# Optimization experiments

Measured on AMD Instinct MI355X. Metric: run time of the kernel, lower is better.

Reference implementation:

```python
import jax, jax.numpy as jnp
import numpy as np

HEADS = 4
DIM_HEAD = 32
GROUPS = 32  # min(256//4, 32)
EPS = 1e-5


def setup_inputs() -> dict:
    key = jax.random.key(0)
    ks = jax.random.split(key, 5)
    B, C, H, W = 16, 256, 64, 64
    CD, HC, WC = 512, 32, 32
    hid = HEADS * DIM_HEAD  # 128
    return {
        "x": jax.random.normal(ks[0], (B, C, H, W), jnp.float32),
        "cond": jax.random.normal(ks[1], (B, CD, HC, WC), jnp.float32),
        "gn_w": jnp.ones((C,), jnp.float32),
        "gn_b": jnp.zeros((C,), jnp.float32),
        "w_q": jax.random.normal(ks[2], (hid, C), jnp.float32) * 0.05,
        "b_q": jnp.zeros((hid,), jnp.float32),
        "w_kv": jax.random.normal(ks[3], (2 * hid, CD), jnp.float32) * 0.05,
        "b_kv": jnp.zeros((2 * hid,), jnp.float32),
        "w_out": jax.random.normal(ks[4], (C, hid), jnp.float32) * 0.05,
        "b_out": jnp.zeros((C,), jnp.float32),
    }


def _group_norm(x, w, b):
    # x: (B, C, H, W); normalize per group over (channels-in-group, H, W)
    B, C, H, W = x.shape
    xg = x.reshape(B, GROUPS, C // GROUPS, H, W)
    mu = jnp.mean(xg, axis=(2, 3, 4), keepdims=True)
    var = jnp.var(xg, axis=(2, 3, 4), keepdims=True)
    xn = ((xg - mu) * jax.lax.rsqrt(var + EPS)).reshape(B, C, H, W)
    return xn * w[None, :, None, None] + b[None, :, None, None]


def _conv1x1(x, w, b):
    # x: (B, Cin, H, W), w: (Cout, Cin), b: (Cout,)
    return jnp.einsum('oc,bchw->bohw', w, x) + b[None, :, None, None]


def reference(x, cond, gn_w, gn_b, w_q, b_q, w_kv, b_kv, w_out, b_out):
    B, C, H, W = x.shape
    hid = HEADS * DIM_HEAD
    xn = _group_norm(x, gn_w, gn_b)
    q = _conv1x1(xn, w_q, b_q)          # (B, hid, H, W)
    kv = _conv1x1(cond, w_kv, b_kv)     # (B, 2*hid, Hc, Wc)
    Nc = kv.shape[2] * kv.shape[3]
    N = H * W
    k = kv[:, :hid].reshape(B, HEADS, DIM_HEAD, Nc)
    v = kv[:, hid:].reshape(B, HEADS, DIM_HEAD, Nc)
    q = q.reshape(B, HEADS, DIM_HEAD, N)
    k = jax.nn.softmax(k, axis=-1)
    # kv outer product: (B, heads, d, e)
    context = jnp.einsum('bhdn,bhen->bhde', k, v)
    # query contraction over d: (B, heads, e, n)
    out = jnp.einsum('bhde,bhdn->bhen', context, q)
    out = out.reshape(B, hid, H, W)
    return _conv1x1(out, w_out, b_out)
```

## Files before the change

kernel.cpp:

```cpp
#include <hip/hip_runtime.h>
#include <hip/hip_bf16.h>

typedef __attribute__((ext_vector_type(8))) short bf16x8;
typedef __attribute__((ext_vector_type(4))) float f32x4;

__device__ __forceinline__ ushort f2bf(float f) {
    __hip_bfloat16 h = __float2bfloat16(f);
    return __builtin_bit_cast(ushort, h);
}
__device__ __forceinline__ unsigned pack2(float a, float b) {
    return (unsigned)f2bf(a) | ((unsigned)f2bf(b) << 16);
}
__device__ __forceinline__ float bflo(unsigned u) { return __uint_as_float(u << 16); }

__global__ __launch_bounds__(512) void kvctx_kernel(const float* __restrict__ w_kv,
                                                    const float* __restrict__ cond,
                                                    const float* __restrict__ b_kv,
                                                    const float* __restrict__ x,
                                                    float* __restrict__ statacc,
                                                    float* __restrict__ rsp,
                                                    float* __restrict__ ctxp) {
    __shared__ ushort lA[256 * 64];
    __shared__ ushort lB[64 * 64];
    __shared__ float scratch[64 * 64];
    __shared__ float red[16];
    int bid = blockIdx.x, t = threadIdx.x;
    if (bid < 256) {
        int b = bid >> 4, nc = bid & 15;
        int col0 = nc * 64;
        int l = t & 63, w = t >> 6;
        int lr = l & 15, lg = l >> 4;
        const float* Bb = cond + (size_t)b * 512 * 1024 + col0;
        int rA = t >> 3, gAr = t & 7, gw = gAr ^ (rA & 7);
        int rB = t >> 4, gB = t & 15;
        int sp = t & 31, sj4 = t >> 5;
        float4 ka0_, ka1_, ka2_, ka3_, ka4_, ka5_, ka6_, ka7_;
        float4 kb0_, kb1_;
#define KC_LOADA(k0) { \
    ka0_ = *(const float4*)&w_kv[(size_t)(rA)       * 512 + (k0) + gAr * 8]; \
    ka1_ = *(const float4*)&w_kv[(size_t)(rA)       * 512 + (k0) + gAr * 8 + 4]; \
    ka2_ = *(const float4*)&w_kv[(size_t)(64 + rA)  * 512 + (k0) + gAr * 8]; \
    ka3_ = *(const float4*)&w_kv[(size_t)(64 + rA)  * 512 + (k0) + gAr * 8 + 4]; \
    ka4_ = *(const float4*)&w_kv[(size_t)(128 + rA) * 512 + (k0) + gAr * 8]; \
    ka5_ = *(const float4*)&w_kv[(size_t)(128 + rA) * 512 + (k0) + gAr * 8 + 4]; \
    ka6_ = *(const float4*)&w_kv[(size_t)(192 + rA) * 512 + (k0) + gAr * 8]; \
    ka7_ = *(const float4*)&w_kv[(size_t)(192 + rA) * 512 + (k0) + gAr * 8 + 4]; }
#define KC_LOADB(k0) { \
    kb0_ = *(const float4*)&Bb[(size_t)((k0) + rB)      * 1024 + gB * 4]; \
    kb1_ = *(const float4*)&Bb[(size_t)((k0) + 32 + rB) * 1024 + gB * 4]; }
#define KC_WRITEA() { uint4 p; \
    p.x = pack2(ka0_.x, ka0_.y); p.y = pack2(ka0_.z, ka0_.w); \
    p.z = pack2(ka1_.x, ka1_.y); p.w = pack2(ka1_.z, ka1_.w); \
    *(uint4*)((char*)lA + (size_t)((rA)       * 8 + gw) * 16) = p; \
    p.x = pack2(ka2_.x, ka2_.y); p.y = pack2(ka2_.z, ka2_.w); \
    p.z = pack2(ka3_.x, ka3_.y); p.w = pack2(ka3_.z, ka3_.w); \
    *(uint4*)((char*)lA + (size_t)((64 + rA)  * 8 + gw) * 16) = p; \
    p.x = pack2(ka4_.x, ka4_.y); p.y = pack2(ka4_.z, ka4_.w); \
    p.z = pack2(ka5_.x, ka5_.y); p.w = pack2(ka5_.z, ka5_.w); \
    *(uint4*)((char*)lA + (size_t)((128 + rA) * 8 + gw) * 16) = p; \
    p.x = pack2(ka6_.x, ka6_.y); p.y = pack2(ka6_.z, ka6_.w); \
    p.z = pack2(ka7_.x, ka7_.y); p.w = pack2(ka7_.z, ka7_.w); \
    *(uint4*)((char*)lA + (size_t)((192 + rA) * 8 + gw) * 16) = p; }
#define KC_WRITEB() { \
    *(float4*)((char*)scratch + (rB)      * 256 + ((gB ^ (((rB)      >> 1) & 15)) * 16)) = kb0_; \
    *(float4*)((char*)scratch + (32 + rB) * 256 + ((gB ^ (((32 + rB) >> 1) & 15)) * 16)) = kb1_; }
#define KC_PACKB() { \
    int swz = sp & 15; \
    float4 s0 = *(const float4*)((char*)scratch + (2*sp)   * 256 + ((sj4 ^ swz) * 16)); \
    float4 s2 = *(const float4*)((char*)scratch + (2*sp+1) * 256 + ((sj4 ^ swz) * 16)); \
    float c0v[4] = {s0.x, s0.y, s0.z, s0.w}; \
    float c1v[4] = {s2.x, s2.y, s2.z, s2.w}; \
    _Pragma("unroll") \
    for (int w4 = 0; w4 < 4; ++w4) { \
        int n = sj4 * 4 + w4; \
        unsigned pk = pack2(c0v[w4], c1v[w4]); \
        *(unsigned*)((char*)lB + n * 128 + (((sp >> 2) ^ (n & 7)) * 16) + (sp & 3) * 4) = pk; \
    } }
        KC_LOADA(0); KC_LOADB(0);
        f32x4 acc[2][4] = {};
        for (int it = 0; it < 8; ++it) {
            KC_WRITEA();
            KC_WRITEB();
            __syncthreads();
            if (it < 7) { KC_LOADA(it * 64 + 64); KC_LOADB(it * 64 + 64); }
            KC_PACKB();
            __syncthreads();
            #pragma unroll
            for (int ks = 0; ks < 2; ++ks) {
                bf16x8 av[2], bv[4];
                #pragma unroll
                for (int mi = 0; mi < 2; ++mi) {
                    int ar = w * 32 + mi * 16 + lr;
                    int q = (ks * 4 + lg) ^ (ar & 7);
                    av[mi] = *(const bf16x8*)((const char*)lA + ar * 128 + q * 16);
                }
                #pragma unroll
                for (int ni = 0; ni < 4; ++ni) {
                    int br = ni * 16 + lr;
                    int q = (ks * 4 + lg) ^ (br & 7);
                    bv[ni] = *(const bf16x8*)((const char*)lB + br * 128 + q * 16);
                }
                #pragma unroll
                for (int mi = 0; mi < 2; ++mi)
                    #pragma unroll
                    for (int ni = 0; ni < 4; ++ni)
                        acc[mi][ni] = __builtin_amdgcn_mfma_f32_16x16x32_bf16(
                            av[mi], bv[ni], acc[mi][ni], 0, 0, 0);
            }
            __syncthreads();
        }
#undef KC_LOADA
#undef KC_LOADB
#undef KC_WRITEA
#undef KC_WRITEB
#undef KC_PACKB
        bool isK = (w < 4);
        float bk[2][4];
        #pragma unroll
        for (int mi = 0; mi < 2; ++mi)
            #pragma unroll
            for (int reg = 0; reg < 4; ++reg)
                bk[mi][reg] = b_kv[w * 32 + mi * 16 + lg * 4 + reg];
        float rs[2][4];
        #pragma unroll
        for (int mi = 0; mi < 2; ++mi)
            #pragma unroll
            for (int reg = 0; reg < 4; ++reg) rs[mi][reg] = 0.f;
        #pragma unroll
        for (int mi = 0; mi < 2; ++mi) {
            #pragma unroll
            for (int ni = 0; ni < 4; ++ni) {
                #pragma unroll
                for (int reg = 0; reg < 4; ++reg) {
                    int R = w * 32 + mi * 16 + lg * 4 + reg;
                    int N = ni * 16 + lr;
                    float val = acc[mi][ni][reg] + bk[mi][reg];
                    ushort uo;
                    if (isK) {
                        uo = f2bf(__expf(val));
                        rs[mi][reg] += bflo((unsigned)uo);
                    } else {
                        uo = f2bf(val);
                    }
                    *(ushort*)((char*)lA + R * 128 + (((N >> 3) ^ (R & 7)) * 16) + (N & 7) * 2) = uo;
                }
            }
        }
        if (isK) {
            #pragma unroll
            for (int mi = 0; mi < 2; ++mi) {
                #pragma unroll
                for (int reg = 0; reg < 4; ++reg) {
                    float v = rs[mi][reg];
                    v += __shfl_xor(v, 1, 64);
                    v += __shfl_xor(v, 2, 64);
                    v += __shfl_xor(v, 4, 64);
                    v += __shfl_xor(v, 8, 64);
                    if (lr == 0)
                        rsp[(size_t)(b * 16 + nc) * 128 + w * 32 + mi * 16 + lg * 4 + reg] = v;
                }
            }
        }
        __syncthreads();
        if (isK) {
            f32x4 c00 = {}, c01 = {}, c10 = {}, c11 = {};
            #pragma unroll
            for (int ks = 0; ks < 2; ++ks) {
                int ar0 = w * 32 + lr,        qa0 = (ks * 4 + lg) ^ (ar0 & 7);
                int ar1 = w * 32 + 16 + lr,   qa1 = (ks * 4 + lg) ^ (ar1 & 7);
                int br0 = 128 + w * 32 + lr,      qb0 = (ks * 4 + lg) ^ (br0 & 7);
                int br1 = 128 + w * 32 + 16 + lr, qb1 = (ks * 4 + lg) ^ (br1 & 7);
                bf16x8 pa0 = *(const bf16x8*)((const char*)lA + ar0 * 128 + qa0 * 16);
                bf16x8 pa1 = *(const bf16x8*)((const char*)lA + ar1 * 128 + qa1 * 16);
                bf16x8 pv0 = *(const bf16x8*)((const char*)lA + br0 * 128 + qb0 * 16);
                bf16x8 pv1 = *(const bf16x8*)((const char*)lA + br1 * 128 + qb1 * 16);
                c00 = __builtin_amdgcn_mfma_f32_16x16x32_bf16(pa0, pv0, c00, 0, 0, 0);
                c01 = __builtin_amdgcn_mfma_f32_16x16x32_bf16(pa0, pv1, c01, 0, 0, 0);
                c10 = __builtin_amdgcn_mfma_f32_16x16x32_bf16(pa1, pv0, c10, 0, 0, 0);
                c11 = __builtin_amdgcn_mfma_f32_16x16x32_bf16(pa1, pv1, c11, 0, 0, 0);
            }
            float* cp = ctxp + (size_t)(b * 16 + nc) * 4096 + w * 1024;
            #pragma unroll
            for (int reg = 0; reg < 4; ++reg) {
                int d0 = lg * 4 + reg;
                cp[d0 * 32 + lr]              = c00[reg];
                cp[d0 * 32 + 16 + lr]         = c01[reg];
                cp[(16 + d0) * 32 + lr]       = c10[reg];
                cp[(16 + d0) * 32 + 16 + lr]  = c11[reg];
            }
        }
    } else {
        int bg = bid - 256;
        const float4* xp = (const float4*)(x + (size_t)bg * 32768);
        float s = 0.f, ss = 0.f;
        #pragma unroll
        for (int j = 0; j < 16; ++j) {
            float4 v = xp[t + 512 * j];
            s  += v.x + v.y + v.z + v.w;
            ss += v.x*v.x + v.y*v.y + v.z*v.z + v.w*v.w;
        }
        #pragma unroll
        for (int off = 32; off > 0; off >>= 1) {
            s  += __shfl_down(s, off, 64);
            ss += __shfl_down(ss, off, 64);
        }
        int wave = t >> 6;
        if ((t & 63) == 0) { red[wave * 2] = s; red[wave * 2 + 1] = ss; }
        __syncthreads();
        if (t == 0) {
            float S = 0.f, SS = 0.f;
            #pragma unroll
            for (int i = 0; i < 8; ++i) { S += red[i * 2]; SS += red[i * 2 + 1]; }
            statacc[bg * 2]     = S;
            statacc[bg * 2 + 1] = SS;
        }
    }
}

__global__ __launch_bounds__(256) void a_kernel(const float* __restrict__ ctxp,
                                                const float* __restrict__ rsp,
                                                const float* __restrict__ w_out,
                                                const float* __restrict__ w_q,
                                                const float* __restrict__ b_q,
                                                const float* __restrict__ statacc,
                                                const float* __restrict__ gn_w,
                                                const float* __restrict__ gn_b,
                                                const float* __restrict__ b_out,
                                                ushort* __restrict__ A16,
                                                float* __restrict__ biasb) {
    __shared__ float ctxl[4][32][33];
    __shared__ float wol[16][128];
    __shared__ float ml[16][128];
    __shared__ float cbuf[256][17];
    __shared__ float pbuf[16][17];
    __shared__ float rsinv[128];
    int b = blockIdx.x >> 4, ot = (blockIdx.x & 15) << 4;
    int t = threadIdx.x;
    if (t < 128) {
        float s = 0.f;
        #pragma unroll
        for (int nc = 0; nc < 16; ++nc)
            s += rsp[(size_t)(b * 16 + nc) * 128 + t];
        rsinv[t] = 1.f / s;
    }
    #pragma unroll
    for (int j = 0; j < 8; ++j) {
        int e = t + 256 * j;
        wol[e >> 7][e & 127] = w_out[(ot + (e >> 7)) * 128 + (e & 127)];
    }
    __syncthreads();
    #pragma unroll
    for (int j = 0; j < 16; ++j) {
        int e = t + 256 * j;
        float v = 0.f;
        #pragma unroll
        for (int nc = 0; nc < 16; ++nc)
            v += ctxp[(size_t)(b * 16 + nc) * 4096 + e];
        ctxl[e >> 10][(e >> 5) & 31][e & 31] = v * rsinv[e >> 5];
    }
    __syncthreads();
    #pragma unroll
    for (int j = 0; j < 8; ++j) {
        int e = t + 256 * j;
        int o = e >> 7, hd = e & 127, h = hd >> 5, d = hd & 31;
        float acc = 0.f;
        #pragma unroll
        for (int ee = 0; ee < 32; ++ee) acc += wol[o][h * 32 + ee] * ctxl[h][d][ee];
        ml[o][hd] = acc;
    }
    __syncthreads();
    int c = t, g = c >> 3;
    float a0 = statacc[(b * 32 + g) * 2], a1 = statacc[(b * 32 + g) * 2 + 1];
    float mu  = a0 * (1.f / 32768.f);
    float var = a1 * (1.f / 32768.f) - mu * mu;
    float sc = rsqrtf(var + 1e-5f) * gn_w[c];
    float tc = gn_b[c] - mu * sc;
    float wt[16];
    #pragma unroll
    for (int o = 0; o < 16; ++o) wt[o] = 0.f;
    for (int hd = 0; hd < 128; ++hd) {
        float wq = w_q[hd * 256 + c];
        #pragma unroll
        for (int o = 0; o < 16; ++o) wt[o] += ml[o][hd] * wq;
    }
    ushort* Abp = A16 + ((size_t)b * 256 + ot) * 256 + c;
    #pragma unroll
    for (int o = 0; o < 16; ++o) {
        Abp[(size_t)o * 256] = f2bf(wt[o] * sc);
        cbuf[c][o] = wt[o] * tc;
    }
    __syncthreads();
    {
        int o = t >> 4, seg = t & 15;
        float p = 0.f;
        #pragma unroll
        for (int i = 0; i < 16; ++i) p += cbuf[seg * 16 + i][o];
        pbuf[o][seg] = p;
    }
    __syncthreads();
    if (t < 16) {
        int o = t;
        float sum = 0.f;
        #pragma unroll
        for (int s2 = 0; s2 < 16; ++s2) sum += pbuf[o][s2];
        float md = 0.f;
        #pragma unroll 8
        for (int hd = 0; hd < 128; ++hd) md += ml[o][hd] * b_q[hd];
        biasb[(size_t)b * 256 + ot + o] = sum + md + b_out[ot + o];
    }
}

__global__ __launch_bounds__(512) void out_gemm_fused(const ushort* __restrict__ A16,
                                                      const float* __restrict__ x,
                                                      const float* __restrict__ biasb,
                                                      float* __restrict__ out) {
    __shared__ ushort lA[256 * 64];
    __shared__ ushort lB[128 * 64];
    __shared__ float scratch[64 * 128];
    int b = blockIdx.y;
    int n0 = blockIdx.x * 128;
    int t = threadIdx.x;
    int l = t & 63, wid = t >> 6;
    int wr = wid >> 1, wc = wid & 1;
    int lr = l & 15, lg = l >> 4;
    const ushort* Ab = A16 + (size_t)b * 65536;
    const float* xb = x + (size_t)b * 256 * 4096 + n0;
    int sp = t & 31, sj = t >> 5;
    uint4 a0_, a1_, a2_, a3_;
    float4 b0_, b1_, b2_, b3_;
    int rA = t >> 3, gA = (t & 7) ^ (rA & 7);
    int rB = t >> 5, gB = t & 31;
#define OG_LOADA(k0) { \
    a0_ = *(const uint4*)(Ab + (size_t)(rA)       * 256 + (k0) + gA * 8); \
    a1_ = *(const uint4*)(Ab + (size_t)(64 + rA)  * 256 + (k0) + gA * 8); \
    a2_ = *(const uint4*)(Ab + (size_t)(128 + rA) * 256 + (k0) + gA * 8); \
    a3_ = *(const uint4*)(Ab + (size_t)(192 + rA) * 256 + (k0) + gA * 8); }
#define OG_LOADB(k0) { \
    b0_ = *(const float4*)&xb[(size_t)((k0) + rB)      * 4096 + gB * 4]; \
    b1_ = *(const float4*)&xb[(size_t)((k0) + 16 + rB) * 4096 + gB * 4]; \
    b2_ = *(const float4*)&xb[(size_t)((k0) + 32 + rB) * 4096 + gB * 4]; \
    b3_ = *(const float4*)&xb[(size_t)((k0) + 48 + rB) * 4096 + gB * 4]; }
    OG_LOADA(0); OG_LOADB(0);
    f32x4 acc[4][4] = {};
    for (int it = 0; it < 4; ++it) {
        *(uint4*)((char*)lA + (size_t)t * 16)          = a0_;
        *(uint4*)((char*)lA + (size_t)(512 + t) * 16)  = a1_;
        *(uint4*)((char*)lA + (size_t)(1024 + t) * 16) = a2_;
        *(uint4*)((char*)lA + (size_t)(1536 + t) * 16) = a3_;
        *(float4*)((char*)scratch + (rB)      * 512 + (gB ^ (((rB)      >> 1) & 31)) * 16) = b0_;
        *(float4*)((char*)scratch + (16 + rB) * 512 + (gB ^ (((16 + rB) >> 1) & 31)) * 16) = b1_;
        *(float4*)((char*)scratch + (32 + rB) * 512 + (gB ^ (((32 + rB) >> 1) & 31)) * 16) = b2_;
        *(float4*)((char*)scratch + (48 + rB) * 512 + (gB ^ (((48 + rB) >> 1) & 31)) * 16) = b3_;
        __syncthreads();
        if (it < 3) { OG_LOADA(it * 64 + 64); OG_LOADB(it * 64 + 64); }
        {
            int swz = sp & 31;
            float4 s0 = *(const float4*)((char*)scratch + (2*sp)   * 512 + ((2*sj)   ^ swz) * 16);
            float4 s1 = *(const float4*)((char*)scratch + (2*sp)   * 512 + ((2*sj+1) ^ swz) * 16);
            float4 s2 = *(const float4*)((char*)scratch + (2*sp+1) * 512 + ((2*sj)   ^ swz) * 16);
            float4 s3 = *(const float4*)((char*)scratch + (2*sp+1) * 512 + ((2*sj+1) ^ swz) * 16);
            float c0v[8] = {s0.x, s0.y, s0.z, s0.w, s1.x, s1.y, s1.z, s1.w};
            float c1v[8] = {s2.x, s2.y, s2.z, s2.w, s3.x, s3.y, s3.z, s3.w};
            #pragma unroll
            for (int w = 0; w < 8; ++w) {
                int n = sj * 8 + w;
                unsigned pk = pack2(c0v[w], c1v[w]);
                *(unsigned*)((char*)lB + n * 128 + (((sp >> 2) ^ (n & 7)) * 16) + (sp & 3) * 4) = pk;
            }
        }
        __syncthreads();
        #pragma unroll
        for (int ks = 0; ks < 2; ++ks) {
            bf16x8 av[4], bv[4];
            #pragma unroll
            for (int mi = 0; mi < 4; ++mi) {
                int ar = wr * 64 + mi * 16 + lr;
                int q = (ks * 4 + lg) ^ (ar & 7);
                av[mi] = *(const bf16x8*)((const char*)lA + ar * 128 + q * 16);
            }
            #pragma unroll
            for (int ni = 0; ni < 4; ++ni) {
                int br = wc * 64 + ni * 16 + lr;
                int q = (ks * 4 + lg) ^ (br & 7);
                bv[ni] = *(const bf16x8*)((const char*)lB + br * 128 + q * 16);
            }
            #pragma unroll
            for (int mi = 0; mi < 4; ++mi)
                #pragma unroll
                for (int ni = 0; ni < 4; ++ni)
                    acc[mi][ni] = __builtin_amdgcn_mfma_f32_16x16x32_bf16(
                        av[mi], bv[ni], acc[mi][ni], 0, 0, 0);
        }
        __syncthreads();
    }
#undef OG_LOADA
#undef OG_LOADB
    const float* bp = biasb + (size_t)b * 256;
    int orow = wr * 64, ocol = n0 + wc * 64 + lr;
    #pragma unroll
    for (int mi = 0; mi < 4; ++mi) {
        int rb = orow + mi * 16 + lg * 4;
        float4 b4 = *(const float4*)&bp[rb];
        float bvr[4] = {b4.x, b4.y, b4.z, b4.w};
        #pragma unroll
        for (int ni = 0; ni < 4; ++ni) {
            int cc = ocol + ni * 16;
            #pragma unroll
            for (int r = 0; r < 4; ++r)
                out[((size_t)b * 256 + rb + r) * 4096 + cc] = acc[mi][ni][r] + bvr[r];
        }
    }
}

extern "C" void kernel_launch(void* const* d_in, const int* in_sizes, int n_in,
                              void* d_out, int out_size, void* d_ws, size_t ws_size,
                              hipStream_t stream) {
    const float* x     = (const float*)d_in[0];
    const float* cond  = (const float*)d_in[1];
    const float* gn_w  = (const float*)d_in[2];
    const float* gn_b  = (const float*)d_in[3];
    const float* w_q   = (const float*)d_in[4];
    const float* b_q   = (const float*)d_in[5];
    const float* w_kv  = (const float*)d_in[6];
    const float* b_kv  = (const float*)d_in[7];
    const float* w_out = (const float*)d_in[8];
    const float* b_out = (const float*)d_in[9];
    float* out = (float*)d_out;

    float* f       = (float*)d_ws;
    float* statacc = f;
    float* rsp     = f + 1024;
    float* ctxp    = f + 33792;
    float* biasb   = f + 1082368;
    ushort* A16    = (ushort*)(f + 1086464);

    kvctx_kernel<<<768, 512, 0, stream>>>(w_kv, cond, b_kv, x, statacc, rsp, ctxp);
    a_kernel<<<256, 256, 0, stream>>>(ctxp, rsp, w_out, w_q, b_q, statacc,
                                      gn_w, gn_b, b_out, A16, biasb);
    out_gemm_fused<<<dim3(32, 16), 512, 0, stream>>>(A16, x, biasb, out);
}
```

Before: 77.89 us.

## Fuse group-norm statistics into KV GEMM blocks, interleaving x loads with MFMA loop

The separate 512 group-norm reduction blocks are removed. Each of the 256 KV/context blocks now also streams two groups of x (64K floats), loading x chunks inside the GEMM k-loop and accumulating sum and sum of squares. The aim is to overlap the memory-bound statistics pass with the compute-bound KV GEMM and to cut the grid from 768 to 256 blocks. In exchange, each block carries more registers and memory traffic, and fewer blocks may leave CUs idle or serialise the x reads behind the GEMM.

```diff
diff --git a/kernel.cpp b/kernel.cpp
--- a/kernel.cpp
+++ b/kernel.cpp
@@ -23,19 +23,21 @@
     __shared__ ushort lA[256 * 64];
     __shared__ ushort lB[64 * 64];
     __shared__ float scratch[64 * 64];
-    __shared__ float red[16];
+    __shared__ float red2[8][4];
     int bid = blockIdx.x, t = threadIdx.x;
-    if (bid < 256) {
-        int b = bid >> 4, nc = bid & 15;
-        int col0 = nc * 64;
-        int l = t & 63, w = t >> 6;
-        int lr = l & 15, lg = l >> 4;
-        const float* Bb = cond + (size_t)b * 512 * 1024 + col0;
-        int rA = t >> 3, gAr = t & 7, gw = gAr ^ (rA & 7);
-        int rB = t >> 4, gB = t & 15;
-        int sp = t & 31, sj4 = t >> 5;
-        float4 ka0_, ka1_, ka2_, ka3_, ka4_, ka5_, ka6_, ka7_;
-        float4 kb0_, kb1_;
+    int b = bid >> 4, nc = bid & 15;
+    int col0 = nc * 64;
+    int l = t & 63, w = t >> 6;
+    int lr = l & 15, lg = l >> 4;
+    const float* Bb = cond + (size_t)b * 512 * 1024 + col0;
+    const float4* xc = (const float4*)(x + (size_t)b * 1048576 + (size_t)nc * 65536);
+    int rA = t >> 3, gAr = t & 7, gw = gAr ^ (rA & 7);
+    int rB = t >> 4, gB = t & 15;
+    int sp = t & 31, sj4 = t >> 5;
+    float4 ka0_, ka1_, ka2_, ka3_, ka4_, ka5_, ka6_, ka7_;
+    float4 kb0_, kb1_;
+    float4 xv0_, xv1_, xv2_, xv3_;
+    float sA = 0.f, ssA = 0.f, sB = 0.f, ssB = 0.f;
 #define KC_LOADA(k0) { \
     ka0_ = *(const float4*)&w_kv[(size_t)(rA)       * 512 + (k0) + gAr * 8]; \
     ka1_ = *(const float4*)&w_kv[(size_t)(rA)       * 512 + (k0) + gAr * 8 + 4]; \
@@ -76,144 +78,155 @@
         unsigned pk = pack2(c0v[w4], c1v[w4]); \
         *(unsigned*)((char*)lB + n * 128 + (((sp >> 2) ^ (n & 7)) * 16) + (sp & 3) * 4) = pk; \
     } }
-        KC_LOADA(0); KC_LOADB(0);
-        f32x4 acc[2][4] = {};
-        for (int it = 0; it < 8; ++it) {
-            KC_WRITEA();
-            KC_WRITEB();
-            __syncthreads();
-            if (it < 7) { KC_LOADA(it * 64 + 64); KC_LOADB(it * 64 + 64); }
-            KC_PACKB();
-            __syncthreads();
-            #pragma unroll
-            for (int ks = 0; ks < 2; ++ks) {
-                bf16x8 av[2], bv[4];
+    KC_LOADA(0); KC_LOADB(0);
+    f32x4 acc[2][4] = {};
+    for (int it = 0; it < 8; ++it) {
+        KC_WRITEA();
+        KC_WRITEB();
+        __syncthreads();
+        if (it < 7) { KC_LOADA(it * 64 + 64); KC_LOADB(it * 64 + 64); }
+        xv0_ = xc[t + 512 * (4 * it)];
+        xv1_ = xc[t + 512 * (4 * it + 1)];
+        xv2_ = xc[t + 512 * (4 * it + 2)];
+        xv3_ = xc[t + 512 * (4 * it + 3)];
+        KC_PACKB();
+        __syncthreads();
+        #pragma unroll
+        for (int ks = 0; ks < 2; ++ks) {
+            bf16x8 av[2], bv[4];
+            #pragma unroll
+            for (int mi = 0; mi < 2; ++mi) {
+                int ar = w * 32 + mi * 16 + lr;
+                int q = (ks * 4 + lg) ^ (ar & 7);
+                av[mi] = *(const bf16x8*)((const char*)lA + ar * 128 + q * 16);
+            }
+            #pragma unroll
+            for (int ni = 0; ni < 4; ++ni) {
+                int br = ni * 16 + lr;
+                int q = (ks * 4 + lg) ^ (br & 7);
+                bv[ni] = *(const bf16x8*)((const char*)lB + br * 128 + q * 16);
+            }
+            #pragma unroll
+            for (int mi = 0; mi < 2; ++mi)
                 #pragma unroll
-                for (int mi = 0; mi < 2; ++mi) {
-                    int ar = w * 32 + mi * 16 + lr;
-                    int q = (ks * 4 + lg) ^ (ar & 7);
-                    av[mi] = *(const bf16x8*)((const char*)lA + ar * 128 + q * 16);
-                }
-                #pragma unroll
-                for (int ni = 0; ni < 4; ++ni) {
-                    int br = ni * 16 + lr;
-                    int q = (ks * 4 + lg) ^ (br & 7);
-                    bv[ni] = *(const bf16x8*)((const char*)lB + br * 128 + q * 16);
-                }
-                #pragma unroll
-                for (int mi = 0; mi < 2; ++mi)
-                    #pragma unroll
-                    for (int ni = 0; ni < 4; ++ni)
-                        acc[mi][ni] = __builtin_amdgcn_mfma_f32_16x16x32_bf16(
-                            av[mi], bv[ni], acc[mi][ni], 0, 0, 0);
-            }
-            __syncthreads();
-        }
+                for (int ni = 0; ni < 4; ++ni)
+                    acc[mi][ni] = __builtin_amdgcn_mfma_f32_16x16x32_bf16(
+                        av[mi], bv[ni], acc[mi][ni], 0, 0, 0);
+        }
+        __syncthreads();
+        float xs = (xv0_.x + xv0_.y + xv0_.z + xv0_.w)
+                 + (xv1_.x + xv1_.y + xv1_.z + xv1_.w)
+                 + (xv2_.x + xv2_.y + xv2_.z + xv2_.w)
+                 + (xv3_.x + xv3_.y + xv3_.z + xv3_.w);
+        float xss = xv0_.x*xv0_.x + xv0_.y*xv0_.y + xv0_.z*xv0_.z + xv0_.w*xv0_.w
+                  + xv1_.x*xv1_.x + xv1_.y*xv1_.y + xv1_.z*xv1_.z + xv1_.w*xv1_.w
+                  + xv2_.x*xv2_.x + xv2_.y*xv2_.y + xv2_.z*xv2_.z + xv2_.w*xv2_.w
+                  + xv3_.x*xv3_.x + xv3_.y*xv3_.y + xv3_.z*xv3_.z + xv3_.w*xv3_.w;
+        if (it < 4) { sA += xs; ssA += xss; } else { sB += xs; ssB += xss; }
+    }
 #undef KC_LOADA
 #undef KC_LOADB
 #undef KC_WRITEA
 #undef KC_WRITEB
 #undef KC_PACKB
-        bool isK = (w < 4);
-        float bk[2][4];
-        #pragma unroll
-        for (int mi = 0; mi < 2; ++mi)
-            #pragma unroll
-            for (int reg = 0; reg < 4; ++reg)
-                bk[mi][reg] = b_kv[w * 32 + mi * 16 + lg * 4 + reg];
-        float rs[2][4];
-        #pragma unroll
-        for (int mi = 0; mi < 2; ++mi)
-            #pragma unroll
-            for (int reg = 0; reg < 4; ++reg) rs[mi][reg] = 0.f;
+    bool isK = (w < 4);
+    float bk[2][4];
+    #pragma unroll
+    for (int mi = 0; mi < 2; ++mi)
+        #pragma unroll
+        for (int reg = 0; reg < 4; ++reg)
+            bk[mi][reg] = b_kv[w * 32 + mi * 16 + lg * 4 + reg];
+    float rs[2][4];
+    #pragma unroll
+    for (int mi = 0; mi < 2; ++mi)
+        #pragma unroll
+        for (int reg = 0; reg < 4; ++reg) rs[mi][reg] = 0.f;
+    #pragma unroll
+    for (int mi = 0; mi < 2; ++mi) {
+        #pragma unroll
+        for (int ni = 0; ni < 4; ++ni) {
+            #pragma unroll
+            for (int reg = 0; reg < 4; ++reg) {
+                int R = w * 32 + mi * 16 + lg * 4 + reg;
+                int N = ni * 16 + lr;
+                float val = acc[mi][ni][reg] + bk[mi][reg];
+                ushort uo;
+                if (isK) {
+                    uo = f2bf(__expf(val));
+                    rs[mi][reg] += bflo((unsigned)uo);
+                } else {
+                    uo = f2bf(val);
+                }
+                *(ushort*)((char*)lA + R * 128 + (((N >> 3) ^ (R & 7)) * 16) + (N & 7) * 2) = uo;
+            }
+        }
+    }
+    if (isK) {
         #pragma unroll
         for (int mi = 0; mi < 2; ++mi) {
             #pragma unroll
-            for (int ni = 0; ni < 4; ++ni) {
-                #pragma unroll
-                for (int reg = 0; reg < 4; ++reg) {
-                    int R = w * 32 + mi * 16 + lg * 4 + reg;
-                    int N = ni * 16 + lr;
-                    float val = acc[mi][ni][reg] + bk[mi][reg];
-                    ushort uo;
-                    if (isK) {
-                        uo = f2bf(__expf(val));
-                        rs[mi][reg] += bflo((unsigned)uo);
-                    } else {
-                        uo = f2bf(val);
-                    }
-                    *(ushort*)((char*)lA + R * 128 + (((N >> 3) ^ (R & 7)) * 16) + (N & 7) * 2) = uo;
-                }
-            }
-        }
-        if (isK) {
-            #pragma unroll
-            for (int mi = 0; mi < 2; ++mi) {
-                #pragma unroll
-                for (int reg = 0; reg < 4; ++reg) {
-                    float v = rs[mi][reg];
-                    v += __shfl_xor(v, 1, 64);
-                    v += __shfl_xor(v, 2, 64);
-                    v += __shfl_xor(v, 4, 64);
-                    v += __shfl_xor(v, 8, 64);
-                    if (lr == 0)
-                        rsp[(size_t)(b * 16 + nc) * 128 + w * 32 + mi * 16 + lg * 4 + reg] = v;
-                }
-            }
-        }
-        __syncthreads();
-        if (isK) {
-            f32x4 c00 = {}, c01 = {}, c10 = {}, c11 = {};
-            #pragma unroll
-            for (int ks = 0; ks < 2; ++ks) {
-                int ar0 = w * 32 + lr,        qa0 = (ks * 4 + lg) ^ (ar0 & 7);
-                int ar1 = w * 32 + 16 + lr,   qa1 = (ks * 4 + lg) ^ (ar1 & 7);
-                int br0 = 128 + w * 32 + lr,      qb0 = (ks * 4 + lg) ^ (br0 & 7);
-                int br1 = 128 + w * 32 + 16 + lr, qb1 = (ks * 4 + lg) ^ (br1 & 7);
-                bf16x8 pa0 = *(const bf16x8*)((const char*)lA + ar0 * 128 + qa0 * 16);
-                bf16x8 pa1 = *(const bf16x8*)((const char*)lA + ar1 * 128 + qa1 * 16);
-                bf16x8 pv0 = *(const bf16x8*)((const char*)lA + br0 * 128 + qb0 * 16);
-                bf16x8 pv1 = *(const bf16x8*)((const char*)lA + br1 * 128 + qb1 * 16);
-                c00 = __builtin_amdgcn_mfma_f32_16x16x32_bf16(pa0, pv0, c00, 0, 0, 0);
-                c01 = __builtin_amdgcn_mfma_f32_16x16x32_bf16(pa0, pv1, c01, 0, 0, 0);
-                c10 = __builtin_amdgcn_mfma_f32_16x16x32_bf16(pa1, pv0, c10, 0, 0, 0);
-                c11 = __builtin_amdgcn_mfma_f32_16x16x32_bf16(pa1, pv1, c11, 0, 0, 0);
-            }
-            float* cp = ctxp + (size_t)(b * 16 + nc) * 4096 + w * 1024;
-            #pragma unroll
             for (int reg = 0; reg < 4; ++reg) {
-                int d0 = lg * 4 + reg;
-                cp[d0 * 32 + lr]              = c00[reg];
-                cp[d0 * 32 + 16 + lr]         = c01[reg];
-                cp[(16 + d0) * 32 + lr]       = c10[reg];
-                cp[(16 + d0) * 32 + 16 + lr]  = c11[reg];
-            }
-        }
-    } else {
-        int bg = bid - 256;
-        const float4* xp = (const float4*)(x + (size_t)bg * 32768);
-        float s = 0.f, ss = 0.f;
-        #pragma unroll
-        for (int j = 0; j < 16; ++j) {
-            float4 v = xp[t + 512 * j];
-            s  += v.x + v.y + v.z + v.w;
-            ss += v.x*v.x + v.y*v.y + v.z*v.z + v.w*v.w;
-        }
-        #pragma unroll
-        for (int off = 32; off > 0; off >>= 1) {
-            s  += __shfl_down(s, off, 64);
-            ss += __shfl_down(ss, off, 64);
-        }
-        int wave = t >> 6;
-        if ((t & 63) == 0) { red[wave * 2] = s; red[wave * 2 + 1] = ss; }
-        __syncthreads();
-        if (t == 0) {
-            float S = 0.f, SS = 0.f;
-            #pragma unroll
-            for (int i = 0; i < 8; ++i) { S += red[i * 2]; SS += red[i * 2 + 1]; }
-            statacc[bg * 2]     = S;
-            statacc[bg * 2 + 1] = SS;
-        }
+                float v = rs[mi][reg];
+                v += __shfl_xor(v, 1, 64);
+                v += __shfl_xor(v, 2, 64);
+                v += __shfl_xor(v, 4, 64);
+                v += __shfl_xor(v, 8, 64);
+                if (lr == 0)
+                    rsp[(size_t)(b * 16 + nc) * 128 + w * 32 + mi * 16 + lg * 4 + reg] = v;
+            }
+        }
+    }
+    __syncthreads();
+    if (isK) {
+        f32x4 c00 = {}, c01 = {}, c10 = {}, c11 = {};
+        #pragma unroll
+        for (int ks = 0; ks < 2; ++ks) {
+            int ar0 = w * 32 + lr,        qa0 = (ks * 4 + lg) ^ (ar0 & 7);
+            int ar1 = w * 32 + 16 + lr,   qa1 = (ks * 4 + lg) ^ (ar1 & 7);
+            int br0 = 128 + w * 32 + lr,      qb0 = (ks * 4 + lg) ^ (br0 & 7);
+            int br1 = 128 + w * 32 + 16 + lr, qb1 = (ks * 4 + lg) ^ (br1 & 7);
+            bf16x8 pa0 = *(const bf16x8*)((const char*)lA + ar0 * 128 + qa0 * 16);
+            bf16x8 pa1 = *(const bf16x8*)((const char*)lA + ar1 * 128 + qa1 * 16);
+            bf16x8 pv0 = *(const bf16x8*)((const char*)lA + br0 * 128 + qb0 * 16);
+            bf16x8 pv1 = *(const bf16x8*)((const char*)lA + br1 * 128 + qb1 * 16);
+            c00 = __builtin_amdgcn_mfma_f32_16x16x32_bf16(pa0, pv0, c00, 0, 0, 0);
+            c01 = __builtin_amdgcn_mfma_f32_16x16x32_bf16(pa0, pv1, c01, 0, 0, 0);
+            c10 = __builtin_amdgcn_mfma_f32_16x16x32_bf16(pa1, pv0, c10, 0, 0, 0);
+            c11 = __builtin_amdgcn_mfma_f32_16x16x32_bf16(pa1, pv1, c11, 0, 0, 0);
+        }
+        float* cp = ctxp + (size_t)(b * 16 + nc) * 4096 + w * 1024;
+        #pragma unroll
+        for (int reg = 0; reg < 4; ++reg) {
+            int d0 = lg * 4 + reg;
+            cp[d0 * 32 + lr]              = c00[reg];
+            cp[d0 * 32 + 16 + lr]         = c01[reg];
+            cp[(16 + d0) * 32 + lr]       = c10[reg];
+            cp[(16 + d0) * 32 + 16 + lr]  = c11[reg];
+        }
+    }
+    #pragma unroll
+    for (int off = 32; off > 0; off >>= 1) {
+        sA  += __shfl_down(sA, off, 64);
+        ssA += __shfl_down(ssA, off, 64);
+        sB  += __shfl_down(sB, off, 64);
+        ssB += __shfl_down(ssB, off, 64);
+    }
+    if ((t & 63) == 0) {
+        red2[w][0] = sA; red2[w][1] = ssA; red2[w][2] = sB; red2[w][3] = ssB;
+    }
+    __syncthreads();
+    if (t == 0) {
+        float S0 = 0.f, SS0 = 0.f, S1 = 0.f, SS1 = 0.f;
+        #pragma unroll
+        for (int i = 0; i < 8; ++i) {
+            S0 += red2[i][0]; SS0 += red2[i][1];
+            S1 += red2[i][2]; SS1 += red2[i][3];
+        }
+        int bg0 = b * 32 + nc * 2;
+        statacc[bg0 * 2]     = S0;
+        statacc[bg0 * 2 + 1] = SS0;
+        statacc[bg0 * 2 + 2] = S1;
+        statacc[bg0 * 2 + 3] = SS1;
     }
 }
 
@@ -434,7 +447,7 @@
     float* biasb   = f + 1082368;
     ushort* A16    = (ushort*)(f + 1086464);
 
-    kvctx_kernel<<<768, 512, 0, stream>>>(w_kv, cond, b_kv, x, statacc, rsp, ctxp);
+    kvctx_kernel<<<256, 512, 0, stream>>>(w_kv, cond, b_kv, x, statacc, rsp, ctxp);
     a_kernel<<<256, 256, 0, stream>>>(ctxp, rsp, w_out, w_q, b_q, statacc,
                                       gn_w, gn_b, b_out, A16, biasb);
     out_gemm_fused<<<dim3(32, 16), 512, 0, stream>>>(A16, x, biasb, out);
```

New measurement: 80.73 us. 3.7% more time.

## Fuse GroupNorm stats into KV-context blocks and halve column tile

Applied to the files above, without the earlier changes.

The KV projection/context kernel now uses 32-column tiles (512 uniform blocks instead of 256 GEMM blocks plus 512 separate stat blocks). Each block also streams its share of x during the GEMM k-loop and reduces the group sum and sum of squares, folding the GroupNorm statistics into the same blocks. This removes the heterogeneous block split and lets the x loads overlap the MFMA work. In exchange, the partial context and row-sum buffers double in size, so the follow-up kernel reduces over 32 partials instead of 16, and the x loads add register pressure to the GEMM loop.

```diff
diff --git a/kernel.cpp b/kernel.cpp
--- a/kernel.cpp
+++ b/kernel.cpp
@@ -21,21 +21,23 @@
                                                     float* __restrict__ rsp,
                                                     float* __restrict__ ctxp) {
     __shared__ ushort lA[256 * 64];
-    __shared__ ushort lB[64 * 64];
-    __shared__ float scratch[64 * 64];
-    __shared__ float red[16];
+    __shared__ ushort lB[32 * 64];
+    __shared__ float scratch[64 * 32];
+    __shared__ float red2[8][2];
     int bid = blockIdx.x, t = threadIdx.x;
-    if (bid < 256) {
-        int b = bid >> 4, nc = bid & 15;
-        int col0 = nc * 64;
-        int l = t & 63, w = t >> 6;
-        int lr = l & 15, lg = l >> 4;
-        const float* Bb = cond + (size_t)b * 512 * 1024 + col0;
-        int rA = t >> 3, gAr = t & 7, gw = gAr ^ (rA & 7);
-        int rB = t >> 4, gB = t & 15;
-        int sp = t & 31, sj4 = t >> 5;
-        float4 ka0_, ka1_, ka2_, ka3_, ka4_, ka5_, ka6_, ka7_;
-        float4 kb0_, kb1_;
+    int b = bid >> 5, nc = bid & 31;
+    int col0 = nc * 32;
+    int l = t & 63, w = t >> 6;
+    int lr = l & 15, lg = l >> 4;
+    const float* Bb = cond + (size_t)b * 512 * 1024 + col0;
+    const float4* xc = (const float4*)(x + (size_t)b * 1048576 + (size_t)nc * 32768);
+    int rA = t >> 3, gAr = t & 7, gw = gAr ^ (rA & 7);
+    int rB = t >> 3, gB = t & 7;
+    int sp = t & 31, sj4 = (t >> 5) & 7;
+    float4 ka0_, ka1_, ka2_, ka3_, ka4_, ka5_, ka6_, ka7_;
+    float4 kb0_;
+    float4 xv0_, xv1_;
+    float sA = 0.f, ssA = 0.f;
 #define KC_LOADA(k0) { \
     ka0_ = *(const float4*)&w_kv[(size_t)(rA)       * 512 + (k0) + gAr * 8]; \
     ka1_ = *(const float4*)&w_kv[(size_t)(rA)       * 512 + (k0) + gAr * 8 + 4]; \
@@ -46,8 +48,7 @@
     ka6_ = *(const float4*)&w_kv[(size_t)(192 + rA) * 512 + (k0) + gAr * 8]; \
     ka7_ = *(const float4*)&w_kv[(size_t)(192 + rA) * 512 + (k0) + gAr * 8 + 4]; }
 #define KC_LOADB(k0) { \
-    kb0_ = *(const float4*)&Bb[(size_t)((k0) + rB)      * 1024 + gB * 4]; \
-    kb1_ = *(const float4*)&Bb[(size_t)((k0) + 32 + rB) * 1024 + gB * 4]; }
+    kb0_ = *(const float4*)&Bb[(size_t)((k0) + rB) * 1024 + gB * 4]; }
 #define KC_WRITEA() { uint4 p; \
     p.x = pack2(ka0_.x, ka0_.y); p.y = pack2(ka0_.z, ka0_.w); \
     p.z = pack2(ka1_.x, ka1_.y); p.w = pack2(ka1_.z, ka1_.w); \
@@ -62,12 +63,11 @@
     p.z = pack2(ka7_.x, ka7_.y); p.w = pack2(ka7_.z, ka7_.w); \
     *(uint4*)((char*)lA + (size_t)((192 + rA) * 8 + gw) * 16) = p; }
 #define KC_WRITEB() { \
-    *(float4*)((char*)scratch + (rB)      * 256 + ((gB ^ (((rB)      >> 1) & 15)) * 16)) = kb0_; \
-    *(float4*)((char*)scratch + (32 + rB) * 256 + ((gB ^ (((32 + rB) >> 1) & 15)) * 16)) = kb1_; }
-#define KC_PACKB() { \
-    int swz = sp & 15; \
-    float4 s0 = *(const float4*)((char*)scratch + (2*sp)   * 256 + ((sj4 ^ swz) * 16)); \
-    float4 s2 = *(const float4*)((char*)scratch + (2*sp+1) * 256 + ((sj4 ^ swz) * 16)); \
+    *(float4*)((char*)scratch + (rB) * 128 + ((gB ^ ((rB >> 1) & 7)) * 16)) = kb0_; }
+#define KC_PACKB() if (t < 256) { \
+    int js = sj4 ^ (sp & 7); \
+    float4 s0 = *(const float4*)((char*)scratch + (2*sp)   * 128 + js * 16); \
+    float4 s2 = *(const float4*)((char*)scratch + (2*sp+1) * 128 + js * 16); \
     float c0v[4] = {s0.x, s0.y, s0.z, s0.w}; \
     float c1v[4] = {s2.x, s2.y, s2.z, s2.w}; \
     _Pragma("unroll") \
@@ -76,144 +76,137 @@
         unsigned pk = pack2(c0v[w4], c1v[w4]); \
         *(unsigned*)((char*)lB + n * 128 + (((sp >> 2) ^ (n & 7)) * 16) + (sp & 3) * 4) = pk; \
     } }
-        KC_LOADA(0); KC_LOADB(0);
-        f32x4 acc[2][4] = {};
-        for (int it = 0; it < 8; ++it) {
-            KC_WRITEA();
-            KC_WRITEB();
-            __syncthreads();
-            if (it < 7) { KC_LOADA(it * 64 + 64); KC_LOADB(it * 64 + 64); }
-            KC_PACKB();
-            __syncthreads();
-            #pragma unroll
-            for (int ks = 0; ks < 2; ++ks) {
-                bf16x8 av[2], bv[4];
+    KC_LOADA(0); KC_LOADB(0);
+    f32x4 acc[2][2] = {};
+    for (int it = 0; it < 8; ++it) {
+        KC_WRITEA();
+        KC_WRITEB();
+        __syncthreads();
+        if (it < 7) { KC_LOADA(it * 64 + 64); KC_LOADB(it * 64 + 64); }
+        xv0_ = xc[t + 512 * (2 * it)];
+        xv1_ = xc[t + 512 * (2 * it + 1)];
+        KC_PACKB();
+        __syncthreads();
+        #pragma unroll
+        for (int ks = 0; ks < 2; ++ks) {
+            bf16x8 av[2], bv[2];
+            #pragma unroll
+            for (int mi = 0; mi < 2; ++mi) {
+                int ar = w * 32 + mi * 16 + lr;
+                int q = (ks * 4 + lg) ^ (ar & 7);
+                av[mi] = *(const bf16x8*)((const char*)lA + ar * 128 + q * 16);
+            }
+            #pragma unroll
+            for (int ni = 0; ni < 2; ++ni) {
+                int br = ni * 16 + lr;
+                int q = (ks * 4 + lg) ^ (br & 7);
+                bv[ni] = *(const bf16x8*)((const char*)lB + br * 128 + q * 16);
+            }
+            #pragma unroll
+            for (int mi = 0; mi < 2; ++mi)
                 #pragma unroll
-                for (int mi = 0; mi < 2; ++mi) {
-                    int ar = w * 32 + mi * 16 + lr;
-                    int q = (ks * 4 + lg) ^ (ar & 7);
-                    av[mi] = *(const bf16x8*)((const char*)lA + ar * 128 + q * 16);
-                }
-                #pragma unroll
-                for (int ni = 0; ni < 4; ++ni) {
-                    int br = ni * 16 + lr;
-                    int q = (ks * 4 + lg) ^ (br & 7);
-                    bv[ni] = *(const bf16x8*)((const char*)lB + br * 128 + q * 16);
-                }
-                #pragma unroll
-                for (int mi = 0; mi < 2; ++mi)
-                    #pragma unroll
-                    for (int ni = 0; ni < 4; ++ni)
-                        acc[mi][ni] = __builtin_amdgcn_mfma_f32_16x16x32_bf16(
-                            av[mi], bv[ni], acc[mi][ni], 0, 0, 0);
-            }
-            __syncthreads();
-        }
+                for (int ni = 0; ni < 2; ++ni)
+                    acc[mi][ni] = __builtin_amdgcn_mfma_f32_16x16x32_bf16(
+                        av[mi], bv[ni], acc[mi][ni], 0, 0, 0);
+        }
+        __syncthreads();
+        float xs = (xv0_.x + xv0_.y + xv0_.z + xv0_.w)
+                 + (xv1_.x + xv1_.y + xv1_.z + xv1_.w);
+        float xss = xv0_.x*xv0_.x + xv0_.y*xv0_.y + xv0_.z*xv0_.z + xv0_.w*xv0_.w
+                  + xv1_.x*xv1_.x + xv1_.y*xv1_.y + xv1_.z*xv1_.z + xv1_.w*xv1_.w;
+        sA += xs; ssA += xss;
+    }
 #undef KC_LOADA
 #undef KC_LOADB
 #undef KC_WRITEA
 #undef KC_WRITEB
 #undef KC_PACKB
-        bool isK = (w < 4);
-        float bk[2][4];
-        #pragma unroll
-        for (int mi = 0; mi < 2; ++mi)
-            #pragma unroll
-            for (int reg = 0; reg < 4; ++reg)
-                bk[mi][reg] = b_kv[w * 32 + mi * 16 + lg * 4 + reg];
-        float rs[2][4];
-        #pragma unroll
-        for (int mi = 0; mi < 2; ++mi)
-            #pragma unroll
-            for (int reg = 0; reg < 4; ++reg) rs[mi][reg] = 0.f;
+    bool isK = (w < 4);
+    float bk[2][4];
+    #pragma unroll
+    for (int mi = 0; mi < 2; ++mi)
+        #pragma unroll
+        for (int reg = 0; reg < 4; ++reg)
+            bk[mi][reg] = b_kv[w * 32 + mi * 16 + lg * 4 + reg];
+    float rs[2][4];
+    #pragma unroll
+    for (int mi = 0; mi < 2; ++mi)
+        #pragma unroll
+        for (int reg = 0; reg < 4; ++reg) rs[mi][reg] = 0.f;
+    #pragma unroll
+    for (int mi = 0; mi < 2; ++mi) {
+        #pragma unroll
+        for (int ni = 0; ni < 2; ++ni) {
+            #pragma unroll
+            for (int reg = 0; reg < 4; ++reg) {
+                int R = w * 32 + mi * 16 + lg * 4 + reg;
+                int N = ni * 16 + lr;
+                float val = acc[mi][ni][reg] + bk[mi][reg];
+                ushort uo;
+                if (isK) {
+                    uo = f2bf(__expf(val));
+                    rs[mi][reg] += bflo((unsigned)uo);
+                } else {
+                    uo = f2bf(val);
+                }
+                *(ushort*)((char*)lA + R * 64 + (((N >> 3) ^ (R & 3)) * 16) + (N & 7) * 2) = uo;
+            }
+        }
+    }
+    if (isK) {
         #pragma unroll
         for (int mi = 0; mi < 2; ++mi) {
             #pragma unroll
-            for (int ni = 0; ni < 4; ++ni) {
-                #pragma unroll
-                for (int reg = 0; reg < 4; ++reg) {
-                    int R = w * 32 + mi * 16 + lg * 4 + reg;
-                    int N = ni * 16 + lr;
-                    float val = acc[mi][ni][reg] + bk[mi][reg];
-                    ushort uo;
-                    if (isK) {
-                        uo = f2bf(__expf(val));
-                        rs[mi][reg] += bflo((unsigned)uo);
-                    } else {
-                        uo = f2bf(val);
-                    }
-                    *(ushort*)((char*)lA + R * 128 + (((N >> 3) ^ (R & 7)) * 16) + (N & 7) * 2) = uo;
-                }
-            }
-        }
-        if (isK) {
-            #pragma unroll
-            for (int mi = 0; mi < 2; ++mi) {
-                #pragma unroll
-                for (int reg = 0; reg < 4; ++reg) {
-                    float v = rs[mi][reg];
-                    v += __shfl_xor(v, 1, 64);
-                    v += __shfl_xor(v, 2, 64);
-                    v += __shfl_xor(v, 4, 64);
-                    v += __shfl_xor(v, 8, 64);
-                    if (lr == 0)
-                        rsp[(size_t)(b * 16 + nc) * 128 + w * 32 + mi * 16 + lg * 4 + reg] = v;
-                }
-            }
-        }
-        __syncthreads();
-        if (isK) {
-            f32x4 c00 = {}, c01 = {}, c10 = {}, c11 = {};
-            #pragma unroll
-            for (int ks = 0; ks < 2; ++ks) {
-                int ar0 = w * 32 + lr,        qa0 = (ks * 4 + lg) ^ (ar0 & 7);
-                int ar1 = w * 32 + 16 + lr,   qa1 = (ks * 4 + lg) ^ (ar1 & 7);
-                int br0 = 128 + w * 32 + lr,      qb0 = (ks * 4 + lg) ^ (br0 & 7);
-                int br1 = 128 + w * 32 + 16 + lr, qb1 = (ks * 4 + lg) ^ (br1 & 7);
-                bf16x8 pa0 = *(const bf16x8*)((const char*)lA + ar0 * 128 + qa0 * 16);
-                bf16x8 pa1 = *(const bf16x8*)((const char*)lA + ar1 * 128 + qa1 * 16);
-                bf16x8 pv0 = *(const bf16x8*)((const char*)lA + br0 * 128 + qb0 * 16);
-                bf16x8 pv1 = *(const bf16x8*)((const char*)lA + br1 * 128 + qb1 * 16);
-                c00 = __builtin_amdgcn_mfma_f32_16x16x32_bf16(pa0, pv0, c00, 0, 0, 0);
-                c01 = __builtin_amdgcn_mfma_f32_16x16x32_bf16(pa0, pv1, c01, 0, 0, 0);
-                c10 = __builtin_amdgcn_mfma_f32_16x16x32_bf16(pa1, pv0, c10, 0, 0, 0);
-                c11 = __builtin_amdgcn_mfma_f32_16x16x32_bf16(pa1, pv1, c11, 0, 0, 0);
-            }
-            float* cp = ctxp + (size_t)(b * 16 + nc) * 4096 + w * 1024;
-            #pragma unroll
             for (int reg = 0; reg < 4; ++reg) {
-                int d0 = lg * 4 + reg;
-                cp[d0 * 32 + lr]              = c00[reg];
-                cp[d0 * 32 + 16 + lr]         = c01[reg];
-                cp[(16 + d0) * 32 + lr]       = c10[reg];
-                cp[(16 + d0) * 32 + 16 + lr]  = c11[reg];
-            }
-        }
-    } else {
-        int bg = bid - 256;
-        const float4* xp = (const float4*)(x + (size_t)bg * 32768);
-        float s = 0.f, ss = 0.f;
-        #pragma unroll
-        for (int j = 0; j < 16; ++j) {
-            float4 v = xp[t + 512 * j];
-            s  += v.x + v.y + v.z + v.w;
-            ss += v.x*v.x + v.y*v.y + v.z*v.z + v.w*v.w;
-        }
-        #pragma unroll
-        for (int off = 32; off > 0; off >>= 1) {
-            s  += __shfl_down(s, off, 64);
-            ss += __shfl_down(ss, off, 64);
-        }
-        int wave = t >> 6;
-        if ((t & 63) == 0) { red[wave * 2] = s; red[wave * 2 + 1] = ss; }
-        __syncthreads();
-        if (t == 0) {
-            float S = 0.f, SS = 0.f;
-            #pragma unroll
-            for (int i = 0; i < 8; ++i) { S += red[i * 2]; SS += red[i * 2 + 1]; }
-            statacc[bg * 2]     = S;
-            statacc[bg * 2 + 1] = SS;
-        }
+                float v = rs[mi][reg];
+                v += __shfl_xor(v, 1, 64);
+                v += __shfl_xor(v, 2, 64);
+                v += __shfl_xor(v, 4, 64);
+                v += __shfl_xor(v, 8, 64);
+                if (lr == 0)
+                    rsp[(size_t)(b * 32 + nc) * 128 + w * 32 + mi * 16 + lg * 4 + reg] = v;
+            }
+        }
+    }
+    __syncthreads();
+    if (isK) {
+        int ar0 = w * 32 + lr,            qa0 = lg ^ (ar0 & 3);
+        int ar1 = w * 32 + 16 + lr,       qa1 = lg ^ (ar1 & 3);
+        int br0 = 128 + w * 32 + lr,      qb0 = lg ^ (br0 & 3);
+        int br1 = 128 + w * 32 + 16 + lr, qb1 = lg ^ (br1 & 3);
+        bf16x8 pa0 = *(const bf16x8*)((const char*)lA + ar0 * 64 + qa0 * 16);
+        bf16x8 pa1 = *(const bf16x8*)((const char*)lA + ar1 * 64 + qa1 * 16);
+        bf16x8 pv0 = *(const bf16x8*)((const char*)lA + br0 * 64 + qb0 * 16);
+        bf16x8 pv1 = *(const bf16x8*)((const char*)lA + br1 * 64 + qb1 * 16);
+        f32x4 c00 = {}, c01 = {}, c10 = {}, c11 = {};
+        c00 = __builtin_amdgcn_mfma_f32_16x16x32_bf16(pa0, pv0, c00, 0, 0, 0);
+        c01 = __builtin_amdgcn_mfma_f32_16x16x32_bf16(pa0, pv1, c01, 0, 0, 0);
+        c10 = __builtin_amdgcn_mfma_f32_16x16x32_bf16(pa1, pv0, c10, 0, 0, 0);
+        c11 = __builtin_amdgcn_mfma_f32_16x16x32_bf16(pa1, pv1, c11, 0, 0, 0);
+        float* cp = ctxp + (size_t)(b * 32 + nc) * 4096 + w * 1024;
+        #pragma unroll
+        for (int reg = 0; reg < 4; ++reg) {
+            int d0 = lg * 4 + reg;
+            cp[d0 * 32 + lr]              = c00[reg];
+            cp[d0 * 32 + 16 + lr]         = c01[reg];
+            cp[(16 + d0) * 32 + lr]       = c10[reg];
+            cp[(16 + d0) * 32 + 16 + lr]  = c11[reg];
+        }
+    }
+    #pragma unroll
+    for (int off = 32; off > 0; off >>= 1) {
+        sA  += __shfl_down(sA, off, 64);
+        ssA += __shfl_down(ssA, off, 64);
+    }
+    if ((t & 63) == 0) { red2[w][0] = sA; red2[w][1] = ssA; }
+    __syncthreads();
+    if (t == 0) {
+        float S = 0.f, SS = 0.f;
+        #pragma unroll
+        for (int i = 0; i < 8; ++i) { S += red2[i][0]; SS += red2[i][1]; }
+        int bg = b * 32 + nc;
+        statacc[bg * 2]     = S;
+        statacc[bg * 2 + 1] = SS;
     }
 }
 
@@ -239,8 +232,8 @@
     if (t < 128) {
         float s = 0.f;
         #pragma unroll
-        for (int nc = 0; nc < 16; ++nc)
-            s += rsp[(size_t)(b * 16 + nc) * 128 + t];
+        for (int nc = 0; nc < 32; ++nc)
+            s += rsp[(size_t)(b * 32 + nc) * 128 + t];
         rsinv[t] = 1.f / s;
     }
     #pragma unroll
@@ -254,8 +247,8 @@
         int e = t + 256 * j;
         float v = 0.f;
         #pragma unroll
-        for (int nc = 0; nc < 16; ++nc)
-            v += ctxp[(size_t)(b * 16 + nc) * 4096 + e];
+        for (int nc = 0; nc < 32; ++nc)
+            v += ctxp[(size_t)(b * 32 + nc) * 4096 + e];
         ctxl[e >> 10][(e >> 5) & 31][e & 31] = v * rsinv[e >> 5];
     }
     __syncthreads();
@@ -430,11 +423,11 @@
     float* f       = (float*)d_ws;
     float* statacc = f;
     float* rsp     = f + 1024;
-    float* ctxp    = f + 33792;
-    float* biasb   = f + 1082368;
-    ushort* A16    = (ushort*)(f + 1086464);
-
-    kvctx_kernel<<<768, 512, 0, stream>>>(w_kv, cond, b_kv, x, statacc, rsp, ctxp);
+    float* ctxp    = f + 66560;
+    float* biasb   = f + 2163712;
+    ushort* A16    = (ushort*)(f + 2167808);
+
+    kvctx_kernel<<<512, 512, 0, stream>>>(w_kv, cond, b_kv, x, statacc, rsp, ctxp);
     a_kernel<<<256, 256, 0, stream>>>(ctxp, rsp, w_out, w_q, b_q, statacc,
                                       gn_w, gn_b, b_out, A16, biasb);
     out_gemm_fused<<<dim3(32, 16), 512, 0, stream>>>(A16, x, biasb, out);
```

Result: slower. 184.1 us (+136.3%).
